# Optimization experiments

Hardware: AMD Instinct MI355X
Metric: run time of the kernel (lower is better)

The kernel has to match this reference:

```python
import jax, jax.numpy as jnp
import numpy as np

D_MODEL = 1024
NUM_HEADS = 16
HEAD_DIM = D_MODEL // NUM_HEADS
WINDOW = 256
NEG = -1000000000.0


def setup_inputs() -> dict:
    key = jax.random.key(0)
    ks = jax.random.split(key, 9)
    B, N, D = 2, 2048, D_MODEL
    s = 1.0 / np.sqrt(D)
    inp = {
        "x": jax.random.normal(ks[0], (B, N, D), dtype=jnp.float32),
        "Wq": jax.random.normal(ks[1], (D, D), dtype=jnp.float32) * s,
        "bq": jnp.zeros((D,), dtype=jnp.float32),
        "Wk": jax.random.normal(ks[2], (D, D), dtype=jnp.float32) * s,
        "bk": jnp.zeros((D,), dtype=jnp.float32),
        "Wv": jax.random.normal(ks[3], (D, D), dtype=jnp.float32) * s,
        "bv": jnp.zeros((D,), dtype=jnp.float32),
        "Wo": jax.random.normal(ks[4], (D, D), dtype=jnp.float32) * s,
        "bo": jnp.zeros((D,), dtype=jnp.float32),
    }
    return inp


def reference(x, Wq, bq, Wk, bk, Wv, bv, Wo, bo):
    B, N, D = x.shape
    H, hd = NUM_HEADS, HEAD_DIM
    q = (x @ Wq + bq).reshape(B, N, H, hd).transpose(0, 2, 1, 3)  # [B,H,N,hd]
    k = (x @ Wk + bk).reshape(B, N, H, hd).transpose(0, 2, 1, 3)
    v = (x @ Wv + bv).reshape(B, N, H, hd).transpose(0, 2, 1, 3)

    i = jnp.arange(N)[:, None]
    j = jnp.arange(N)[None, :]
    blocked = (j > i) | (j < i - WINDOW)  # causal + local window
    mask = jnp.where(blocked, jnp.float32(NEG), jnp.float32(0.0))  # [N,N]

    logits = jnp.einsum("bhid,bhjd->bhij", q, k) / jnp.sqrt(jnp.float32(hd))
    logits = logits + mask[None, None, :, :]
    attn = jax.nn.softmax(logits, axis=-1)
    out = jnp.einsum("bhij,bhjd->bhid", attn, v)  # [B,H,N,hd]
    out = out.transpose(0, 2, 1, 3).reshape(B, N, D)
    return out @ Wo + bo
```

## Files before the change

### kernel.cpp

```cpp
#include <hip/hip_runtime.h>


typedef unsigned short ushort_t;
typedef __bf16 bf16x8 __attribute__((ext_vector_type(8)));
typedef float f32x4 __attribute__((ext_vector_type(4)));
typedef unsigned short ushort8 __attribute__((ext_vector_type(8)));
typedef unsigned short ushort4v __attribute__((ext_vector_type(4)));

#define LOG2E 1.4426950408889634f

static __device__ __forceinline__ ushort_t f2b(float f) {
    union { float f; unsigned int u; } x;
    x.f = f;
    unsigned int u = x.u;
    unsigned int r = (u + 0x7FFFu + ((u >> 16) & 1u)) >> 16;
    return (ushort_t)r;
}

static __device__ __forceinline__ void store_out(float* p, float v) { *p = v; }
static __device__ __forceinline__ void store_out(ushort_t* p, float v) { *p = f2b(v); }

static __device__ __forceinline__ int sw(int row, int c) {
    return (row * 8 + (c ^ (row & 7))) * 8;
}

static __device__ __forceinline__ void gload_lds16(const ushort_t* g, ushort_t* l) {
    __builtin_amdgcn_global_load_lds(
        (const __attribute__((address_space(1))) void*)g,
        (__attribute__((address_space(3))) void*)l, 16, 0, 0);
}

__global__ __launch_bounds__(256) void prep_kernel(
    const float* __restrict__ x, ushort_t* __restrict__ xbf,
    const float* __restrict__ W0, const float* __restrict__ W1,
    const float* __restrict__ W2, const float* __restrict__ W3,
    ushort_t* __restrict__ T0, ushort_t* __restrict__ T1,
    ushort_t* __restrict__ T2, ushort_t* __restrict__ T3) {
    int tx = threadIdx.x, ty = threadIdx.y;
    if (blockIdx.z == 4) {
        int idx = (blockIdx.y * 32 + blockIdx.x) * 256 + ty * 32 + tx;
        int i = idx * 16;
#pragma unroll
        for (int half = 0; half < 2; half++) {
            f32x4 a = *(const f32x4*)&x[i + half * 8];
            f32x4 b = *(const f32x4*)&x[i + half * 8 + 4];
            ushort8 o;
#pragma unroll
            for (int e = 0; e < 4; e++) o[e] = f2b(a[e]);
#pragma unroll
            for (int e = 0; e < 4; e++) o[4 + e] = f2b(b[e]);
            *(ushort8*)&xbf[i + half * 8] = o;
        }
        return;
    }
    __shared__ ushort_t tile[32][33];
    const float* W;
    ushort_t* T;
    switch (blockIdx.z) {
        case 0: W = W0; T = T0; break;
        case 1: W = W1; T = T1; break;
        case 2: W = W2; T = T2; break;
        default: W = W3; T = T3; break;
    }
    int xx = blockIdx.x * 32 + tx;
    int ybase = blockIdx.y * 32 + ty;
#pragma unroll
    for (int r = 0; r < 4; r++) tile[ty + r * 8][tx] = f2b(W[(ybase + r * 8) * 1024 + xx]);
    __syncthreads();
    {
        int u = ty * 32 + tx;
        int ro = u >> 3;
        int cg = (u & 7) * 4;
        ushort4v o;
#pragma unroll
        for (int k = 0; k < 4; k++) o[k] = tile[cg + k][ro];
        *(ushort4v*)&T[(long)(blockIdx.x * 32 + ro) * 1024 + blockIdx.y * 32 + cg] = o;
    }
}

__global__ __launch_bounds__(256) void gemm_qkv_kernel(
    const ushort_t* __restrict__ A,
    const ushort_t* __restrict__ Bt0, const ushort_t* __restrict__ Bt1,
    const ushort_t* __restrict__ Bt2,
    const float* __restrict__ bias0, const float* __restrict__ bias1,
    const float* __restrict__ bias2,
    ushort_t* __restrict__ C0, ushort_t* __restrict__ C1, ushort_t* __restrict__ C2,
    float os0, float os1, float os2) {
    __shared__ ushort_t Al[64 * 64];
    __shared__ ushort_t Bl[128 * 64];

    const int id = blockIdx.x;
    const int xcd = id & 7;
    const int s = id >> 3;
    int m_blk = (xcd >> 1) * 16 + (s & 15);
    int ncol = (xcd & 1) * 12 + (s >> 4);
    int zsel = ncol >> 3;
    ncol &= 7;
    const int m0 = m_blk * 64;
    const int n0 = ncol * 128;

    const ushort_t* Bt;
    const float* bias;
    ushort_t* C;
    float oscale;
    if (zsel == 0) { Bt = Bt0; bias = bias0; C = C0; oscale = os0; }
    else if (zsel == 1) { Bt = Bt1; bias = bias1; C = C1; oscale = os1; }
    else { Bt = Bt2; bias = bias2; C = C2; oscale = os2; }

    const int tid = threadIdx.x;
    const int w = tid >> 6;
    const int l = tid & 63;
    const int wm = (w >> 1) * 32;
    const int wn = (w & 1) * 64;
    const int lrow = l & 15;
    const int lq = l >> 4;

    f32x4 acc[2][4];
#pragma unroll
    for (int mi = 0; mi < 2; mi++)
#pragma unroll
        for (int ni = 0; ni < 4; ni++) acc[mi][ni] = 0.0f;

    const int kt0 = (id * 5) & 15;
    for (int it = 0; it < 16; it++) {
        const int kt = ((kt0 + it) & 15) * 64;
#pragma unroll
        for (int t = 0; t < 2; t++) {
            int idx = t * 256 + tid;
            int row = idx >> 3, cs = idx & 7, c = cs ^ (row & 7);
            gload_lds16(&A[(long)(m0 + row) * 1024 + kt + c * 8], &Al[idx * 8]);
        }
#pragma unroll
        for (int t = 0; t < 4; t++) {
            int idx = t * 256 + tid;
            int row = idx >> 3, cs = idx & 7, c = cs ^ (row & 7);
            gload_lds16(&Bt[(long)(n0 + row) * 1024 + kt + c * 8], &Bl[idx * 8]);
        }
        __syncthreads();
#pragma unroll
        for (int ks = 0; ks < 64; ks += 32) {
            const int cb = (ks >> 3) + lq;
            bf16x8 af[2], bfr[4];
#pragma unroll
            for (int mi = 0; mi < 2; mi++)
                af[mi] = *(const bf16x8*)&Al[sw(wm + mi * 16 + lrow, cb)];
#pragma unroll
            for (int ni = 0; ni < 4; ni++)
                bfr[ni] = *(const bf16x8*)&Bl[sw(wn + ni * 16 + lrow, cb)];
#pragma unroll
            for (int mi = 0; mi < 2; mi++)
#pragma unroll
                for (int ni = 0; ni < 4; ni++)
                    acc[mi][ni] = __builtin_amdgcn_mfma_f32_16x16x32_bf16(
                        af[mi], bfr[ni], acc[mi][ni], 0, 0, 0);
        }
        __syncthreads();
    }

    if (zsel == 2) {
#pragma unroll
        for (int ni = 0; ni < 4; ni++) {
            int n = n0 + wn + ni * 16 + lrow;
            float bv = bias[n];
#pragma unroll
            for (int mi = 0; mi < 2; mi++) {
                int m = m0 + wm + mi * 16 + lq * 4;
                ushort4v o;
#pragma unroll
                for (int r = 0; r < 4; r++) o[r] = f2b((acc[mi][ni][r] + bv) * oscale);
                *(ushort4v*)&C[(long)n * 4096 + m] = o;
            }
        }
    } else {
#pragma unroll
        for (int ni = 0; ni < 4; ni++) {
            int n = n0 + wn + ni * 16 + lrow;
            float bv = bias[n];
#pragma unroll
            for (int mi = 0; mi < 2; mi++) {
#pragma unroll
                for (int r = 0; r < 4; r++) {
                    int m = m0 + wm + mi * 16 + lq * 4 + r;
                    store_out(&C[(long)m * 1024 + n], (acc[mi][ni][r] + bv) * oscale);
                }
            }
        }
    }
}

__global__ __launch_bounds__(256) void gemm_out_kernel(
    const ushort_t* __restrict__ A, const ushort_t* __restrict__ Bt,
    const float* __restrict__ bias, float* __restrict__ C) {
    __shared__ ushort_t Al[64 * 64];
    __shared__ ushort_t Bl[128 * 64];

    const int id = blockIdx.x;
    const int xcd = id & 7;
    const int s = id >> 3;
    const int m_blk = xcd * 8 + (s & 7);
    const int ncol = s >> 3;
    const int m0 = m_blk * 64;
    const int n0 = ncol * 128;

    const int tid = threadIdx.x;
    const int w = tid >> 6;
    const int l = tid & 63;
    const int wm = (w >> 1) * 32;
    const int wn = (w & 1) * 64;
    const int lrow = l & 15;
    const int lq = l >> 4;

    f32x4 acc[2][4];
#pragma unroll
    for (int mi = 0; mi < 2; mi++)
#pragma unroll
        for (int ni = 0; ni < 4; ni++) acc[mi][ni] = 0.0f;

    const int kt0 = (id * 5) & 15;
    for (int it = 0; it < 16; it++) {
        const int kt = ((kt0 + it) & 15) * 64;
#pragma unroll
        for (int t = 0; t < 2; t++) {
            int idx = t * 256 + tid;
            int row = idx >> 3, cs = idx & 7, c = cs ^ (row & 7);
            gload_lds16(&A[(long)(m0 + row) * 1024 + kt + c * 8], &Al[idx * 8]);
        }
#pragma unroll
        for (int t = 0; t < 4; t++) {
            int idx = t * 256 + tid;
            int row = idx >> 3, cs = idx & 7, c = cs ^ (row & 7);
            gload_lds16(&Bt[(long)(n0 + row) * 1024 + kt + c * 8], &Bl[idx * 8]);
        }
        __syncthreads();
#pragma unroll
        for (int ks = 0; ks < 64; ks += 32) {
            const int cb = (ks >> 3) + lq;
            bf16x8 af[2], bfr[4];
#pragma unroll
            for (int mi = 0; mi < 2; mi++)
                af[mi] = *(const bf16x8*)&Al[sw(wm + mi * 16 + lrow, cb)];
#pragma unroll
            for (int ni = 0; ni < 4; ni++)
                bfr[ni] = *(const bf16x8*)&Bl[sw(wn + ni * 16 + lrow, cb)];
#pragma unroll
            for (int mi = 0; mi < 2; mi++)
#pragma unroll
                for (int ni = 0; ni < 4; ni++)
                    acc[mi][ni] = __builtin_amdgcn_mfma_f32_16x16x32_bf16(
                        af[mi], bfr[ni], acc[mi][ni], 0, 0, 0);
        }
        __syncthreads();
    }

#pragma unroll
    for (int ni = 0; ni < 4; ni++) {
        int n = n0 + wn + ni * 16 + lrow;
        float bv = bias[n];
#pragma unroll
        for (int mi = 0; mi < 2; mi++) {
#pragma unroll
            for (int r = 0; r < 4; r++) {
                int m = m0 + wm + mi * 16 + lq * 4 + r;
                C[(long)m * 1024 + n] = acc[mi][ni][r] + bv;
            }
        }
    }
}

__global__ __launch_bounds__(256) void attn_kernel(
    const ushort_t* __restrict__ Q, const ushort_t* __restrict__ K,
    const ushort_t* __restrict__ VT, ushort_t* __restrict__ O) {
    __shared__ ushort_t Kl[128 * 64];
    __shared__ ushort_t Vtl[64 * 128];
    __shared__ ushort_t Pb[4 * 16 * 40];

    const int id = blockIdx.x;
    const int xcd = id & 7;
    const int s = id >> 3;
    const int bh = xcd * 4 + (s >> 5);
    const int b = bh >> 4;
    const int h = bh & 15;
    const int i0 = (s & 31) * 64;

    const int tid = threadIdx.x;
    const int w = tid >> 6;
    const int l = tid & 63;
    const int lrow = l & 15;
    const int lq = l >> 4;
    const int q0 = i0 + w * 16;

    const long baseBH = ((long)b * 2048) * 1024 + (long)h * 64;
    const long baseVT = (long)h * 64 * 4096 + (long)b * 2048;

    const ushort_t* qrow = Q + baseBH + (long)(q0 + lrow) * 1024;
    bf16x8 aq0 = *(const bf16x8*)&qrow[lq * 8];
    bf16x8 aq1 = *(const bf16x8*)&qrow[32 + lq * 8];

    float lpart[4];
    f32x4 oacc[4];
#pragma unroll
    for (int r = 0; r < 4; r++) lpart[r] = 0.0f;
#pragma unroll
    for (int ni = 0; ni < 4; ni++) oacc[ni] = 0.0f;

    const int kstart = (i0 - 256) > 0 ? (i0 - 256) : 0;
    const int kend = i0 + 64;
    ushort_t* Pw = &Pb[w * 16 * 40];

    for (int cs = kstart; cs < kend; cs += 128) {
        const int ce = (cs + 128 < kend) ? cs + 128 : kend;
#pragma unroll
        for (int t = 0; t < 4; t++) {
            int idx = t * 256 + tid;
            int rr = idx >> 3;
            int cc = idx & 7;
            int c = cc ^ (rr & 7);
            int key = cs + rr;
            key = key < 2047 ? key : 2047;
            gload_lds16(&K[baseBH + (long)key * 1024 + c * 8], &Kl[idx * 8]);
        }
#pragma unroll
        for (int t = 0; t < 4; t++) {
            int idx = t * 256 + tid;
            int rr = idx >> 4;
            int cc = idx & 15;
            int c = (cc & 8) | ((cc & 7) ^ (rr & 7));
            int kc = cs + c * 8;
            kc = kc < 2040 ? kc : 2040;
            gload_lds16(&VT[baseVT + (long)rr * 4096 + kc], &Vtl[idx * 8]);
        }
        __syncthreads();

        for (int kb = cs; kb < ce; kb += 32) {
            if (kb > q0 + 15 || kb + 31 < q0 - 256) continue;
            const int rb = kb - cs;
            f32x4 S0 = 0.0f, S1 = 0.0f;
            {
                bf16x8 bk;
                bk = *(const bf16x8*)&Kl[sw(rb + lrow, lq)];
                S0 = __builtin_amdgcn_mfma_f32_16x16x32_bf16(aq0, bk, S0, 0, 0, 0);
                bk = *(const bf16x8*)&Kl[sw(rb + lrow, 4 + lq)];
                S0 = __builtin_amdgcn_mfma_f32_16x16x32_bf16(aq1, bk, S0, 0, 0, 0);
                bk = *(const bf16x8*)&Kl[sw(rb + 16 + lrow, lq)];
                S1 = __builtin_amdgcn_mfma_f32_16x16x32_bf16(aq0, bk, S1, 0, 0, 0);
                bk = *(const bf16x8*)&Kl[sw(rb + 16 + lrow, 4 + lq)];
                S1 = __builtin_amdgcn_mfma_f32_16x16x32_bf16(aq1, bk, S1, 0, 0, 0);
            }
            const int col0 = kb + lrow;
            const int col1 = kb + 16 + lrow;
#pragma unroll
            for (int r = 0; r < 4; r++) {
                const int i = q0 + lq * 4 + r;
                float p0 = (col0 > i || col0 < i - 256) ? 0.0f : exp2f(S0[r] * LOG2E);
                float p1 = (col1 > i || col1 < i - 256) ? 0.0f : exp2f(S1[r] * LOG2E);
                lpart[r] += p0 + p1;
                const int prow = lq * 4 + r;
                Pw[prow * 40 + lrow] = f2b(p0);
                Pw[prow * 40 + 16 + lrow] = f2b(p1);
            }
            bf16x8 pf = *(const bf16x8*)&Pw[lrow * 40 + lq * 8];
#pragma unroll
            for (int ni = 0; ni < 4; ni++) {
                int ccg = (rb >> 3) + lq;
                int rsw = (ccg & 8) | ((ccg & 7) ^ (lrow & 7));
                bf16x8 vf = *(const bf16x8*)&Vtl[(ni * 16 + lrow) * 128 + rsw * 8];
                oacc[ni] = __builtin_amdgcn_mfma_f32_16x16x32_bf16(pf, vf, oacc[ni], 0, 0, 0);
            }
        }
        __syncthreads();
    }

    float lS[4];
#pragma unroll
    for (int r = 0; r < 4; r++) {
        float rs = lpart[r];
#pragma unroll
        for (int off = 8; off; off >>= 1) rs += __shfl_xor(rs, off, 64);
        lS[r] = rs;
    }

#pragma unroll
    for (int ni = 0; ni < 4; ni++) {
#pragma unroll
        for (int r = 0; r < 4; r++) {
            const int i = q0 + lq * 4 + r;
            const int d = ni * 16 + lrow;
            O[baseBH + (long)i * 1024 + d] = f2b(oacc[ni][r] / lS[r]);
        }
    }
}

extern "C" void kernel_launch(void* const* d_in, const int* in_sizes, int n_in,
                              void* d_out, int out_size, void* d_ws, size_t ws_size,
                              hipStream_t stream) {
    const float* x  = (const float*)d_in[0];
    const float* Wq = (const float*)d_in[1];
    const float* bq = (const float*)d_in[2];
    const float* Wk = (const float*)d_in[3];
    const float* bk = (const float*)d_in[4];
    const float* Wv = (const float*)d_in[5];
    const float* bv = (const float*)d_in[6];
    const float* Wo = (const float*)d_in[7];
    const float* bo = (const float*)d_in[8];
    float* out = (float*)d_out;

    ushort_t* ws = (ushort_t*)d_ws;
    const size_t WMAT = (size_t)1024 * 1024;
    const size_t ACT = (size_t)2 * 2048 * 1024;
    ushort_t* xbf = ws;
    ushort_t* Wqt = xbf + ACT;
    ushort_t* Wkt = Wqt + WMAT;
    ushort_t* Wvt = Wkt + WMAT;
    ushort_t* Wot = Wvt + WMAT;
    ushort_t* qws = Wot + WMAT;
    ushort_t* kws = qws + ACT;
    ushort_t* vws = kws + ACT;
    ushort_t* aws = xbf;

    prep_kernel<<<dim3(32, 32, 5), dim3(32, 8), 0, stream>>>(
        x, xbf, Wq, Wk, Wv, Wo, Wqt, Wkt, Wvt, Wot);

    gemm_qkv_kernel<<<1536, 256, 0, stream>>>(
        xbf, Wqt, Wkt, Wvt, bq, bk, bv, qws, kws, vws, 0.125f, 1.0f, 1.0f);

    attn_kernel<<<1024, 256, 0, stream>>>(qws, kws, vws, aws);

    gemm_out_kernel<<<512, 256, 0, stream>>>(aws, Wot, bo, out);
}
```

Baseline: 163.1 us.

## Compute transposed score tiles so P stays in registers, skipping LDS round-trip

Swaps the MFMA operand order so each lane holds scores for one query row across keys. The probabilities then feed the PV MFMA directly from registers instead of being staged through a shared-memory buffer. V fragments are gathered with two 4-element LDS reads to match the permuted key ordering. Masking is skipped for fully interior key blocks, and the output is written with 4-wide vector stores after a single reciprocal.

```diff
diff --git a/kernel.cpp b/kernel.cpp
--- a/kernel.cpp
+++ b/kernel.cpp
@@ -272,7 +272,6 @@
     const ushort_t* __restrict__ VT, ushort_t* __restrict__ O) {
     __shared__ ushort_t Kl[128 * 64];
     __shared__ ushort_t Vtl[64 * 128];
-    __shared__ ushort_t Pb[4 * 16 * 40];
 
     const int id = blockIdx.x;
     const int xcd = id & 7;
@@ -296,16 +295,14 @@
     bf16x8 aq0 = *(const bf16x8*)&qrow[lq * 8];
     bf16x8 aq1 = *(const bf16x8*)&qrow[32 + lq * 8];
 
-    float lpart[4];
+    const int q = q0 + lrow;
+    float lpart = 0.0f;
     f32x4 oacc[4];
-#pragma unroll
-    for (int r = 0; r < 4; r++) lpart[r] = 0.0f;
 #pragma unroll
     for (int ni = 0; ni < 4; ni++) oacc[ni] = 0.0f;
 
     const int kstart = (i0 - 256) > 0 ? (i0 - 256) : 0;
     const int kend = i0 + 64;
-    ushort_t* Pw = &Pb[w * 16 * 40];
 
     for (int cs = kstart; cs < kend; cs += 128) {
         const int ce = (cs + 128 < kend) ? cs + 128 : kend;
@@ -336,57 +333,71 @@
             const int rb = kb - cs;
             f32x4 S0 = 0.0f, S1 = 0.0f;
             {
-                bf16x8 bk;
-                bk = *(const bf16x8*)&Kl[sw(rb + lrow, lq)];
-                S0 = __builtin_amdgcn_mfma_f32_16x16x32_bf16(aq0, bk, S0, 0, 0, 0);
-                bk = *(const bf16x8*)&Kl[sw(rb + lrow, 4 + lq)];
-                S0 = __builtin_amdgcn_mfma_f32_16x16x32_bf16(aq1, bk, S0, 0, 0, 0);
-                bk = *(const bf16x8*)&Kl[sw(rb + 16 + lrow, lq)];
-                S1 = __builtin_amdgcn_mfma_f32_16x16x32_bf16(aq0, bk, S1, 0, 0, 0);
-                bk = *(const bf16x8*)&Kl[sw(rb + 16 + lrow, 4 + lq)];
-                S1 = __builtin_amdgcn_mfma_f32_16x16x32_bf16(aq1, bk, S1, 0, 0, 0);
-            }
-            const int col0 = kb + lrow;
-            const int col1 = kb + 16 + lrow;
-#pragma unroll
-            for (int r = 0; r < 4; r++) {
-                const int i = q0 + lq * 4 + r;
-                float p0 = (col0 > i || col0 < i - 256) ? 0.0f : exp2f(S0[r] * LOG2E);
-                float p1 = (col1 > i || col1 < i - 256) ? 0.0f : exp2f(S1[r] * LOG2E);
-                lpart[r] += p0 + p1;
-                const int prow = lq * 4 + r;
-                Pw[prow * 40 + lrow] = f2b(p0);
-                Pw[prow * 40 + 16 + lrow] = f2b(p1);
-            }
-            bf16x8 pf = *(const bf16x8*)&Pw[lrow * 40 + lq * 8];
-#pragma unroll
-            for (int ni = 0; ni < 4; ni++) {
-                int ccg = (rb >> 3) + lq;
-                int rsw = (ccg & 8) | ((ccg & 7) ^ (lrow & 7));
-                bf16x8 vf = *(const bf16x8*)&Vtl[(ni * 16 + lrow) * 128 + rsw * 8];
-                oacc[ni] = __builtin_amdgcn_mfma_f32_16x16x32_bf16(pf, vf, oacc[ni], 0, 0, 0);
-            }
-        }
-        __syncthreads();
-    }
-
-    float lS[4];
-#pragma unroll
-    for (int r = 0; r < 4; r++) {
-        float rs = lpart[r];
-#pragma unroll
-        for (int off = 8; off; off >>= 1) rs += __shfl_xor(rs, off, 64);
-        lS[r] = rs;
-    }
+                bf16x8 bk00 = *(const bf16x8*)&Kl[sw(rb + lrow, lq)];
+                bf16x8 bk01 = *(const bf16x8*)&Kl[sw(rb + lrow, 4 + lq)];
+                bf16x8 bk10 = *(const bf16x8*)&Kl[sw(rb + 16 + lrow, lq)];
+                bf16x8 bk11 = *(const bf16x8*)&Kl[sw(rb + 16 + lrow, 4 + lq)];
+                S0 = __builtin_amdgcn_mfma_f32_16x16x32_bf16(bk00, aq0, S0, 0, 0, 0);
+                S0 = __builtin_amdgcn_mfma_f32_16x16x32_bf16(bk01, aq1, S0, 0, 0, 0);
+                S1 = __builtin_amdgcn_mfma_f32_16x16x32_bf16(bk10, aq0, S1, 0, 0, 0);
+                S1 = __builtin_amdgcn_mfma_f32_16x16x32_bf16(bk11, aq1, S1, 0, 0, 0);
+            }
+            ushort8 pb;
+            if (kb <= q0 - 31 && kb >= q0 - 241) {
+#pragma unroll
+                for (int r = 0; r < 4; r++) {
+                    float p0 = exp2f(S0[r] * LOG2E);
+                    float p1 = exp2f(S1[r] * LOG2E);
+                    lpart += p0 + p1;
+                    pb[r] = f2b(p0);
+                    pb[4 + r] = f2b(p1);
+                }
+            } else {
+#pragma unroll
+                for (int r = 0; r < 4; r++) {
+                    const int key0 = kb + lq * 4 + r;
+                    const int key1 = key0 + 16;
+                    float p0 = (key0 > q || key0 < q - 256) ? 0.0f : exp2f(S0[r] * LOG2E);
+                    float p1 = (key1 > q || key1 < q - 256) ? 0.0f : exp2f(S1[r] * LOG2E);
+                    lpart += p0 + p1;
+                    pb[r] = f2b(p0);
+                    pb[4 + r] = f2b(p1);
+                }
+            }
+            bf16x8 pf = *(bf16x8*)&pb;
+            {
+                const int g1 = (rb >> 3) + (lq >> 1);
+                const int o1 = (lq & 1) * 4;
+                const int g2 = g1 + 2;
+#pragma unroll
+                for (int ni = 0; ni < 4; ni++) {
+                    const int row = ni * 16 + lrow;
+                    const int s1 = (g1 & 8) | ((g1 & 7) ^ (lrow & 7));
+                    const int s2 = (g2 & 8) | ((g2 & 7) ^ (lrow & 7));
+                    ushort4v vlo = *(const ushort4v*)&Vtl[row * 128 + s1 * 8 + o1];
+                    ushort4v vhi = *(const ushort4v*)&Vtl[row * 128 + s2 * 8 + o1];
+                    ushort8 vv;
+#pragma unroll
+                    for (int j = 0; j < 4; j++) { vv[j] = vlo[j]; vv[4 + j] = vhi[j]; }
+                    oacc[ni] = __builtin_amdgcn_mfma_f32_16x16x32_bf16(
+                        *(bf16x8*)&vv, pf, oacc[ni], 0, 0, 0);
+                }
+            }
+        }
+        __syncthreads();
+    }
+
+    float rs = lpart;
+    rs += __shfl_xor(rs, 16, 64);
+    rs += __shfl_xor(rs, 32, 64);
+    const float inv = 1.0f / rs;
 
 #pragma unroll
     for (int ni = 0; ni < 4; ni++) {
-#pragma unroll
-        for (int r = 0; r < 4; r++) {
-            const int i = q0 + lq * 4 + r;
-            const int d = ni * 16 + lrow;
-            O[baseBH + (long)i * 1024 + d] = f2b(oacc[ni][r] / lS[r]);
-        }
+        ushort4v o;
+#pragma unroll
+        for (int r = 0; r < 4; r++) o[r] = f2b(oacc[ni][r] * inv);
+        *(ushort4v*)&O[baseBH + (long)q * 1024 + ni * 16 + lq * 4] = o;
     }
 }
 
```

Measured after the change: 167.7 us. 1.03x slower.
